# Kernel tuning notes

Hardware: AMD Instinct MI355X
Metric: run time of the kernel (lower is better)

Reference implementation:

```python
import jax, jax.numpy as jnp
import numpy as np

B, C, T, F, D, S = 16, 128, 64, 128, 2, 62  # batch, w_dim, seq_in, feat, dilation, seq_out


def setup_inputs() -> dict:
    key = jax.random.key(0)
    ks = jax.random.split(key, 9)
    x = jax.random.normal(ks[0], (B, C, T, F), dtype=jnp.float32)
    # depthwise (2,1) dilated conv params: weight[c, tap]
    w_tanh = jax.random.normal(ks[1], (C, 2), dtype=jnp.float32) * 0.5
    b_tanh = jax.random.normal(ks[2], (C,), dtype=jnp.float32) * 0.1
    w_sig = jax.random.normal(ks[3], (C, 2), dtype=jnp.float32) * 0.5
    b_sig = jax.random.normal(ks[4], (C,), dtype=jnp.float32) * 0.1
    # depthwise 1x1 out conv: one scalar weight + bias per channel
    w_out = jax.random.normal(ks[5], (C,), dtype=jnp.float32) * 0.5
    b_out = jax.random.normal(ks[6], (C,), dtype=jnp.float32) * 0.1
    # residual Linear(seq_in=T -> seq_out=S)
    w_res = jax.random.normal(ks[7], (S, T), dtype=jnp.float32) * (1.0 / np.sqrt(T))
    b_res = jax.random.normal(ks[8], (S,), dtype=jnp.float32) * 0.1
    return {"x": x, "w_tanh": w_tanh, "b_tanh": b_tanh, "w_sig": w_sig,
            "b_sig": b_sig, "w_out": w_out, "b_out": b_out,
            "w_res": w_res, "b_res": b_res, "dilation": D}


def reference(x, w_tanh, b_tanh, w_sig, b_sig, w_out, b_out, w_res, b_res, dilation):
    d = dilation
    # depthwise dilated conv, kernel (2,1): out[t] = w[0]*x[t] + w[1]*x[t+d]
    x0 = x[:, :, : x.shape[2] - d, :]          # [B,C,S,F]
    x1 = x[:, :, d:, :]                         # [B,C,S,F]
    cexp = lambda v: v[None, :, None, None]
    xt = x0 * cexp(w_tanh[:, 0]) + x1 * cexp(w_tanh[:, 1]) + cexp(b_tanh)
    xs = x0 * cexp(w_sig[:, 0]) + x1 * cexp(w_sig[:, 1]) + cexp(b_sig)
    gate = jnp.tanh(xt) * jax.nn.sigmoid(xs)    # [B,C,S,F]
    # residual: Linear over T, output laid out as [B,C,S,F]
    res = jnp.einsum('bctf,st->bcsf', x, w_res) + b_res[None, None, :, None]
    # depthwise 1x1 conv
    out = (gate + res) * cexp(w_out) + cexp(b_out)
    return out
```

## Files before the change

kernel.cpp:

```cpp
#include <hip/hip_runtime.h>


typedef __attribute__((ext_vector_type(8)))  short short8;
typedef __attribute__((ext_vector_type(4)))  float f32x4;
typedef __attribute__((ext_vector_type(4)))  int   i32x4;
typedef __attribute__((ext_vector_type(2)))  float f32x2;

constexpr int Bc = 16, Cc = 128, Tc = 64, Fc = 128, Sc = 62, DIL = 2;
constexpr int LDSW    = 130;
constexpr int LDSROWS = 66;

__device__ inline unsigned cvt_pk_bf16(float lo, float hi) {
    unsigned r;
    asm("v_cvt_pk_bf16_f32 %0, %1, %2" : "=v"(r) : "v"(lo), "v"(hi));
    return r;
}

__global__ __launch_bounds__(256, 4)
void gated_mfma_kernel(const float* __restrict__ x,
                       const float* __restrict__ w_tanh,
                       const float* __restrict__ b_tanh,
                       const float* __restrict__ w_sig,
                       const float* __restrict__ b_sig,
                       const float* __restrict__ w_out,
                       const float* __restrict__ b_out,
                       const float* __restrict__ w_res,
                       const float* __restrict__ b_res,
                       float* __restrict__ out)
{
    __shared__ float lds[LDSROWS * LDSW];

    const int bc   = blockIdx.x;
    const int c    = bc & (Cc - 1);
    const int tid  = threadIdx.x;
    const int lane = tid & 63;
    const int w    = tid >> 6;
    const int g    = lane >> 4;
    const int r16  = lane & 15;

    const float wt0 = w_tanh[2 * c + 0], wt1 = w_tanh[2 * c + 1], bt = b_tanh[c];
    const float ws0 = w_sig[2 * c + 0],  ws1 = w_sig[2 * c + 1],  bs = b_sig[c];
    const float wo  = w_out[c],          bo  = b_out[c];

    const float* xp = x + (size_t)bc * (Tc * Fc);
#pragma unroll
    for (int i = 0; i < 8; ++i) {
        const int o   = tid * 4 + i * 1024;
        const int t   = o >> 7;
        const int col = o & 127;
        const f32x4 v = *(const f32x4*)(xp + o);
        float* d = lds + t * LDSW + col;
        *(f32x2*)(d + 0) = f32x2{v.x, v.y};
        *(f32x2*)(d + 2) = f32x2{v.z, v.w};
    }

    short8 A[4][2];
#pragma unroll
    for (int rt = 0; rt < 4; ++rt) {
        const int row = 16 * rt + r16;
        const bool ok = row < Sc;
        const float* wr = w_res + row * Tc + 8 * g;
#pragma unroll
        for (int kt = 0; kt < 2; ++kt) {
            f32x4 v0 = f32x4{0.f, 0.f, 0.f, 0.f};
            f32x4 v1 = f32x4{0.f, 0.f, 0.f, 0.f};
            if (ok) {
                v0 = *(const f32x4*)(wr + 32 * kt);
                v1 = *(const f32x4*)(wr + 32 * kt + 4);
            }
            const unsigned p0 = cvt_pk_bf16(v0.x, v0.y);
            const unsigned p1 = cvt_pk_bf16(v0.z, v0.w);
            const unsigned p2 = cvt_pk_bf16(v1.x, v1.y);
            const unsigned p3 = cvt_pk_bf16(v1.z, v1.w);
            A[rt][kt] = __builtin_bit_cast(short8,
                          i32x4{(int)p0, (int)p1, (int)p2, (int)p3});
        }
    }

    f32x4 acc[4][2];
#pragma unroll
    for (int rt = 0; rt < 4; ++rt) {
        f32x4 bv;
#pragma unroll
        for (int j = 0; j < 4; ++j) {
            const int idx = 16 * rt + 4 * g + j;
            bv[j] = b_res[idx < Sc ? idx : Sc - 1];
        }
        acc[rt][0] = bv;
        acc[rt][1] = bv;
    }

    __syncthreads();

    const int col0 = 32 * w + r16;
#pragma unroll
    for (int kt = 0; kt < 2; ++kt) {
        short8 Bf[2];
#pragma unroll
        for (int ct = 0; ct < 2; ++ct) {
            const float* bp = lds + (32 * kt + 8 * g) * LDSW + col0 + 16 * ct;
            const unsigned p0 = cvt_pk_bf16(bp[0 * LDSW], bp[1 * LDSW]);
            const unsigned p1 = cvt_pk_bf16(bp[2 * LDSW], bp[3 * LDSW]);
            const unsigned p2 = cvt_pk_bf16(bp[4 * LDSW], bp[5 * LDSW]);
            const unsigned p3 = cvt_pk_bf16(bp[6 * LDSW], bp[7 * LDSW]);
            Bf[ct] = __builtin_bit_cast(short8, i32x4{(int)p0, (int)p1, (int)p2, (int)p3});
        }
#pragma unroll
        for (int rt = 0; rt < 4; ++rt)
#pragma unroll
            for (int ct = 0; ct < 2; ++ct)
                acc[rt][ct] = __builtin_amdgcn_mfma_f32_16x16x32_bf16(
                    A[rt][kt], Bf[ct], acc[rt][ct], 0, 0, 0);
    }

    float* op = out + (size_t)bc * (Sc * Fc);
#pragma unroll
    for (int rt = 0; rt < 4; ++rt) {
        const int r0 = 16 * rt + 4 * g;
#pragma unroll
        for (int ct = 0; ct < 2; ++ct) {
            const int col = col0 + 16 * ct;
            const float* bp = lds + r0 * LDSW + col;
            const float t0 = bp[0 * LDSW];
            const float t1 = bp[1 * LDSW];
            const float t2 = bp[2 * LDSW];
            const float t3 = bp[3 * LDSW];
            const float t4 = bp[4 * LDSW];
            const float t5 = bp[5 * LDSW];

#define GATE_OUT(reg, xa, xb)                                                     \
            if (r0 + (reg) < Sc) {                                                \
                const float xt  = fmaf((xa), wt0, fmaf((xb), wt1, bt));           \
                const float xsg = fmaf((xa), ws0, fmaf((xb), ws1, bs));           \
                const float e2  = __expf(2.0f * xt);                              \
                const float em  = __expf(-xsg);                                   \
                const float gate = (e2 - 1.0f) *                                  \
                    __builtin_amdgcn_rcpf((e2 + 1.0f) * (1.0f + em));             \
                op[(r0 + (reg)) * Fc + col] =                                     \
                    fmaf(gate + acc[rt][ct][reg], wo, bo);                        \
            }
            GATE_OUT(0, t0, t2)
            GATE_OUT(1, t1, t3)
            GATE_OUT(2, t2, t4)
            GATE_OUT(3, t3, t5)
#undef GATE_OUT
        }
    }
}

extern "C" void kernel_launch(void* const* d_in, const int* in_sizes, int n_in,
                              void* d_out, int out_size, void* d_ws, size_t ws_size,
                              hipStream_t stream)
{
    const float* x      = (const float*)d_in[0];
    const float* w_tanh = (const float*)d_in[1];
    const float* b_tanh = (const float*)d_in[2];
    const float* w_sig  = (const float*)d_in[3];
    const float* b_sig  = (const float*)d_in[4];
    const float* w_out  = (const float*)d_in[5];
    const float* b_out  = (const float*)d_in[6];
    const float* w_res  = (const float*)d_in[7];
    const float* b_res  = (const float*)d_in[8];

    float* out = (float*)d_out;

    gated_mfma_kernel<<<Bc * Cc, 256, 0, stream>>>(
        x, w_tanh, b_tanh, w_sig, b_sig, w_out, b_out, w_res, b_res, out);
}
```

Baseline: 33.62 us.

## Stage x as transposed swizzled bf16 in LDS and share w_res fragments

Each thread now loads x, converts it to bf16 once and writes it to LDS transposed (feature-major) with an XOR swizzle. MFMA B fragments then become single 16-byte LDS reads instead of eight scalar reads plus conversions. The w_res A fragments are converted once cooperatively and staged through LDS instead of each wave reading them from global memory. The smaller LDS footprint lets the launch bound rise to 5 blocks per CU. The trade-off is that the gate path now reads bf16-rounded x instead of fp32, which lowers accuracy of the tanh/sigmoid inputs.

```diff
diff --git a/kernel.cpp b/kernel.cpp
--- a/kernel.cpp
+++ b/kernel.cpp
@@ -4,11 +4,13 @@
 typedef __attribute__((ext_vector_type(8)))  short short8;
 typedef __attribute__((ext_vector_type(4)))  float f32x4;
 typedef __attribute__((ext_vector_type(4)))  int   i32x4;
-typedef __attribute__((ext_vector_type(2)))  float f32x2;
+typedef __attribute__((ext_vector_type(2)))  int   i32x2;
 
 constexpr int Bc = 16, Cc = 128, Tc = 64, Fc = 128, Sc = 62, DIL = 2;
-constexpr int LDSW    = 130;
-constexpr int LDSROWS = 66;
+constexpr int LDSTW    = 72;
+constexpr int XT_BYTES = Fc * LDSTW * 2;
+constexpr int A_BYTES  = 8 * 64 * 16;
+constexpr int LDS_TOT  = XT_BYTES + A_BYTES;
 
 __device__ inline unsigned cvt_pk_bf16(float lo, float hi) {
     unsigned r;
@@ -16,7 +18,10 @@
     return r;
 }
 
-__global__ __launch_bounds__(256, 4)
+__device__ inline float bf16_lo(int u) { return __uint_as_float(((unsigned)u) << 16); }
+__device__ inline float bf16_hi(int u) { return __uint_as_float(((unsigned)u) & 0xFFFF0000u); }
+
+__global__ __launch_bounds__(256, 5)
 void gated_mfma_kernel(const float* __restrict__ x,
                        const float* __restrict__ w_tanh,
                        const float* __restrict__ b_tanh,
@@ -28,7 +33,9 @@
                        const float* __restrict__ b_res,
                        float* __restrict__ out)
 {
-    __shared__ float lds[LDSROWS * LDSW];
+    __shared__ i32x4 smem[LDS_TOT / 16];
+    char* lds_base = (char*)smem;
+    char* lds_a    = lds_base + XT_BYTES;
 
     const int bc   = blockIdx.x;
     const int c    = bc & (Cc - 1);
@@ -42,39 +49,43 @@
     const float ws0 = w_sig[2 * c + 0],  ws1 = w_sig[2 * c + 1],  bs = b_sig[c];
     const float wo  = w_out[c],          bo  = b_out[c];
 
+    const int fq = tid & 31;
+    const int tg = tid >> 5;
     const float* xp = x + (size_t)bc * (Tc * Fc);
+    f32x4 v[8];
 #pragma unroll
-    for (int i = 0; i < 8; ++i) {
-        const int o   = tid * 4 + i * 1024;
-        const int t   = o >> 7;
-        const int col = o & 127;
-        const f32x4 v = *(const f32x4*)(xp + o);
-        float* d = lds + t * LDSW + col;
-        *(f32x2*)(d + 0) = f32x2{v.x, v.y};
-        *(f32x2*)(d + 2) = f32x2{v.z, v.w};
+    for (int u = 0; u < 8; ++u)
+        v[u] = *(const f32x4*)(xp + (8 * tg + u) * Fc + 4 * fq);
+
+#pragma unroll
+    for (int i = 0; i < 2; ++i) {
+        const int u   = tid + 256 * i;
+        const int row = u >> 3;
+        const int k8  = u & 7;
+        f32x4 a0 = f32x4{0.f, 0.f, 0.f, 0.f};
+        f32x4 a1 = f32x4{0.f, 0.f, 0.f, 0.f};
+        if (row < Sc) {
+            const float* wr = w_res + row * Tc + 8 * k8;
+            a0 = *(const f32x4*)(wr);
+            a1 = *(const f32x4*)(wr + 4);
+        }
+        const unsigned p0 = cvt_pk_bf16(a0.x, a0.y);
+        const unsigned p1 = cvt_pk_bf16(a0.z, a0.w);
+        const unsigned p2 = cvt_pk_bf16(a1.x, a1.y);
+        const unsigned p3 = cvt_pk_bf16(a1.z, a1.w);
+        const int slot = ((row >> 4) * 2 + (k8 >> 2)) * 64 + (k8 & 3) * 16 + (row & 15);
+        *(i32x4*)(lds_a + slot * 16) = i32x4{(int)p0, (int)p1, (int)p2, (int)p3};
     }
 
-    short8 A[4][2];
+    const int tsw = 8 * (tg ^ (fq & 3));
 #pragma unroll
-    for (int rt = 0; rt < 4; ++rt) {
-        const int row = 16 * rt + r16;
-        const bool ok = row < Sc;
-        const float* wr = w_res + row * Tc + 8 * g;
-#pragma unroll
-        for (int kt = 0; kt < 2; ++kt) {
-            f32x4 v0 = f32x4{0.f, 0.f, 0.f, 0.f};
-            f32x4 v1 = f32x4{0.f, 0.f, 0.f, 0.f};
-            if (ok) {
-                v0 = *(const f32x4*)(wr + 32 * kt);
-                v1 = *(const f32x4*)(wr + 32 * kt + 4);
-            }
-            const unsigned p0 = cvt_pk_bf16(v0.x, v0.y);
-            const unsigned p1 = cvt_pk_bf16(v0.z, v0.w);
-            const unsigned p2 = cvt_pk_bf16(v1.x, v1.y);
-            const unsigned p3 = cvt_pk_bf16(v1.z, v1.w);
-            A[rt][kt] = __builtin_bit_cast(short8,
-                          i32x4{(int)p0, (int)p1, (int)p2, (int)p3});
-        }
+    for (int fj = 0; fj < 4; ++fj) {
+        const unsigned p0 = cvt_pk_bf16(v[0][fj], v[1][fj]);
+        const unsigned p1 = cvt_pk_bf16(v[2][fj], v[3][fj]);
+        const unsigned p2 = cvt_pk_bf16(v[4][fj], v[5][fj]);
+        const unsigned p3 = cvt_pk_bf16(v[6][fj], v[7][fj]);
+        *(i32x4*)(lds_base + ((4 * fq + fj) * LDSTW + tsw) * 2) =
+            i32x4{(int)p0, (int)p1, (int)p2, (int)p3};
     }
 
     f32x4 acc[4][2];
@@ -92,19 +103,22 @@
 
     __syncthreads();
 
+    short8 A[4][2];
+#pragma unroll
+    for (int rt = 0; rt < 4; ++rt)
+#pragma unroll
+        for (int kt = 0; kt < 2; ++kt)
+            A[rt][kt] = *(const short8*)(lds_a + ((rt * 2 + kt) * 64 + lane) * 16);
+
     const int col0 = 32 * w + r16;
+    const int swz8 = 8 * (g ^ (r16 >> 2));
 #pragma unroll
     for (int kt = 0; kt < 2; ++kt) {
         short8 Bf[2];
 #pragma unroll
-        for (int ct = 0; ct < 2; ++ct) {
-            const float* bp = lds + (32 * kt + 8 * g) * LDSW + col0 + 16 * ct;
-            const unsigned p0 = cvt_pk_bf16(bp[0 * LDSW], bp[1 * LDSW]);
-            const unsigned p1 = cvt_pk_bf16(bp[2 * LDSW], bp[3 * LDSW]);
-            const unsigned p2 = cvt_pk_bf16(bp[4 * LDSW], bp[5 * LDSW]);
-            const unsigned p3 = cvt_pk_bf16(bp[6 * LDSW], bp[7 * LDSW]);
-            Bf[ct] = __builtin_bit_cast(short8, i32x4{(int)p0, (int)p1, (int)p2, (int)p3});
-        }
+        for (int ct = 0; ct < 2; ++ct)
+            Bf[ct] = *(const short8*)(lds_base +
+                        ((col0 + 16 * ct) * LDSTW + 32 * kt + swz8) * 2);
 #pragma unroll
         for (int rt = 0; rt < 4; ++rt)
 #pragma unroll
@@ -113,6 +127,7 @@
                     A[rt][kt], Bf[ct], acc[rt][ct], 0, 0, 0);
     }
 
+    const int sw8 = 8 * (r16 >> 2);
     float* op = out + (size_t)bc * (Sc * Fc);
 #pragma unroll
     for (int rt = 0; rt < 4; ++rt) {
@@ -120,13 +135,14 @@
 #pragma unroll
         for (int ct = 0; ct < 2; ++ct) {
             const int col = col0 + 16 * ct;
-            const float* bp = lds + r0 * LDSW + col;
-            const float t0 = bp[0 * LDSW];
-            const float t1 = bp[1 * LDSW];
-            const float t2 = bp[2 * LDSW];
-            const float t3 = bp[3 * LDSW];
-            const float t4 = bp[4 * LDSW];
-            const float t5 = bp[5 * LDSW];
+            const i32x2 d1 = *(const i32x2*)(lds_base + (col * LDSTW + (r0 ^ sw8)) * 2);
+            const i32x2 d2 = *(const i32x2*)(lds_base + (col * LDSTW + ((r0 + 4) ^ sw8)) * 2);
+            const float t0 = bf16_lo(d1.x);
+            const float t1 = bf16_hi(d1.x);
+            const float t2 = bf16_lo(d1.y);
+            const float t3 = bf16_hi(d1.y);
+            const float t4 = bf16_lo(d2.x);
+            const float t5 = bf16_hi(d2.x);
 
 #define GATE_OUT(reg, xa, xb)                                                     \
             if (r0 + (reg) < Sc) {                                                \
```

Result: faster. 27.55 us, median of 3 (-18.1%).
